# Optimization experiments

Hardware: AMD Instinct MI355X
Metric: run time of the kernel (lower is better)

## Reference

```python
import jax, jax.numpy as jnp
import numpy as np

B = 65536      # num_agents * num_processes
NUM = 16       # num_entities (landmarks tracked per agent)


def setup_inputs() -> dict:
    key = jax.random.key(0)
    k = jax.random.split(key, 6)
    value = jax.random.normal(k[0], (B, NUM * 2), jnp.float32)          # last abs positions
    vel = jax.random.normal(k[1], (B, NUM * 2), jnp.float32) * 0.1     # kalman velocities
    A = jax.random.normal(k[2], (B, NUM, 4, 4), jnp.float32) * 0.5
    P = A @ jnp.swapaxes(A, -1, -2) + jnp.eye(4, dtype=jnp.float32) * 0.1  # PSD covariances
    obs = jax.random.normal(k[3], (B, NUM * 2), jnp.float32)            # observed abs positions
    lm = jax.random.randint(k[4], (B, NUM), 0, 8, jnp.int32)            # last-mask age counters
    mask = jax.random.randint(k[5], (B, NUM), 0, 2, jnp.int32)          # current visibility
    return {"value": value, "vel": vel, "P": P, "obs": obs, "lm": lm, "mask": mask}


def _forward(value, vel, P, obs, lm, mask):
    Bn, two_num = value.shape
    num = two_num // 2
    # ---- _infer: constant-velocity predict (dt = 1). NOTE: original code builds Q
    # but never adds it to predicted_P, so we faithfully omit it too.
    Fm = jnp.array([[1., 0., 1., 0.],
                    [0., 1., 0., 1.],
                    [0., 0., 1., 0.],
                    [0., 0., 0., 1.]], jnp.float32)
    states = jnp.concatenate([value.reshape(Bn, num, 2), vel.reshape(Bn, num, 2)], axis=-1)  # [B,n,4]
    pred = jnp.einsum('ij,bnj->bni', Fm, states)                 # F @ state
    pP = jnp.einsum('ij,bnjk,lk->bnil', Fm, P, Fm)               # F P F^T  [B,n,4,4]
    lv = pred[..., :2]
    lvel = pred[..., 2:]
    obs2 = obs.reshape(Bn, num, 2)

    # ---- _merge_tensor: Kalman update with H = [[1,0,0,0],[0,1,0,0]], R = 1e-5 I
    R = jnp.float32(1e-5)
    S = pP[..., :2, :2] + R * jnp.eye(2, dtype=jnp.float32)      # [B,n,2,2]
    det = S[..., 0, 0] * S[..., 1, 1] - S[..., 0, 1] * S[..., 1, 0]
    Sinv = jnp.stack([jnp.stack([S[..., 1, 1], -S[..., 0, 1]], -1),
                      jnp.stack([-S[..., 1, 0], S[..., 0, 0]], -1)], -2) / det[..., None, None]
    K = jnp.einsum('bnij,bnjk->bnik', pP[..., :, :2], Sinv)      # P H^T S^-1  [B,n,4,2]
    y = obs2 - lv                                                # innovation
    upd = pred + jnp.einsum('bnij,bnj->bni', K, y)               # [B,n,4]
    Pn = pP - jnp.einsum('bnij,bnjk->bnik', K, pP[..., :2, :])   # (I - K H) P

    # ---- _fuse condition logic (faithful, including the original's rP bugs:
    # rP for cond2 and cond3b is never written -> stays zero)
    lmf = lm.astype(jnp.float32)
    mf = mask.astype(jnp.float32)
    c1 = (lmf == 0) & (mf == 0)
    c2 = (lmf == 0) & (mf != 0)
    c3 = (lmf != 0) & (mf == 0)
    c4 = (lmf != 0) & (mf != 0)
    c3a = c3 & (lmf <= 5)
    c3e, c4e, c3ae = c3[..., None], c4[..., None], c3a[..., None]
    rv = jnp.where(c4e, upd[..., :2], jnp.where(c3e, lv, obs2))
    rvel = jnp.where(c4e, upd[..., 2:], jnp.where(c3ae, lvel, 0.))
    rm = jnp.where(c2 | c4, 1., jnp.where(c3a, lmf + 1., 0.))
    diagP = jnp.diag(jnp.array([1., 1., 10., 10.], jnp.float32))
    rP = jnp.where(c1[..., None, None], diagP,
                   jnp.where(c3a[..., None, None], pP,
                             jnp.where(c4[..., None, None], Pn, 0.)))
    return rv.reshape(Bn, -1), rm, rvel.reshape(Bn, -1), rP


def reference(value, vel, P, obs, lm, mask):
    return _forward(value, vel, P, obs, lm, mask)
```

## Files before the change

### kernel.cpp

```cpp
#include <hip/hip_runtime.h>

#define NUM 16
#define TPB 256
#define PSTRIDE 20

__global__ __launch_bounds__(TPB) void kf_update_kernel(
    const float* __restrict__ value,
    const float* __restrict__ vel,
    const float* __restrict__ Pin,
    const float* __restrict__ obs,
    const int*   __restrict__ lm,
    const int*   __restrict__ mask,
    float* __restrict__ out,
    int Bn)
{
    __shared__ float sm[TPB * PSTRIDE];

    const int tid   = threadIdx.x;
    const int gtid  = blockIdx.x * TPB + tid;
    const int total = Bn * NUM;
    const long long blockBase = (long long)blockIdx.x * TPB;
    const bool active = gtid < total;

    {
        const float4* Pg = reinterpret_cast<const float4*>(Pin) + blockBase * 4;
        const long long limit = (long long)total * 4 - blockBase * 4;
        #pragma unroll
        for (int k = 0; k < 4; ++k) {
            const int g = tid + TPB * k;
            if (g < limit) {
                const float4 x = Pg[g];
                const int tr = g >> 2, part = g & 3;
                *reinterpret_cast<float4*>(&sm[tr * PSTRIDE + part * 4]) = x;
            }
        }
    }

    float2 v = make_float2(0.f, 0.f), u = v, o = v;
    int l = 0, m = 0;
    if (active) {
        v = reinterpret_cast<const float2*>(value)[gtid];
        u = reinterpret_cast<const float2*>(vel)[gtid];
        o = reinterpret_cast<const float2*>(obs)[gtid];
        l = lm[gtid];
        m = mask[gtid];
    }

    __syncthreads();

    float Pm[16];
    #pragma unroll
    for (int c = 0; c < 4; ++c) {
        const float4 x = *reinterpret_cast<const float4*>(&sm[tid * PSTRIDE + c * 4]);
        Pm[c * 4 + 0] = x.x; Pm[c * 4 + 1] = x.y;
        Pm[c * 4 + 2] = x.z; Pm[c * 4 + 3] = x.w;
    }

    const float p0 = v.x + u.x;
    const float p1 = v.y + u.y;
    const float p2 = u.x;
    const float p3 = u.y;

    float Q[4][4];
    #pragma unroll
    for (int j = 0; j < 4; ++j) {
        Q[0][j] = Pm[0 * 4 + j] + Pm[2 * 4 + j];
        Q[1][j] = Pm[1 * 4 + j] + Pm[3 * 4 + j];
        Q[2][j] = Pm[2 * 4 + j];
        Q[3][j] = Pm[3 * 4 + j];
    }
    float pP[4][4];
    #pragma unroll
    for (int i = 0; i < 4; ++i) {
        pP[i][0] = Q[i][0] + Q[i][2];
        pP[i][1] = Q[i][1] + Q[i][3];
        pP[i][2] = Q[i][2];
        pP[i][3] = Q[i][3];
    }

    const float S00 = pP[0][0] + 1e-5f;
    const float S01 = pP[0][1];
    const float S10 = pP[1][0];
    const float S11 = pP[1][1] + 1e-5f;
    const float det  = S00 * S11 - S01 * S10;
    const float rdet = 1.0f / det;

    float K0[4], K1[4];
    #pragma unroll
    for (int i = 0; i < 4; ++i) {
        K0[i] = (pP[i][0] * S11 - pP[i][1] * S10) * rdet;
        K1[i] = (pP[i][1] * S00 - pP[i][0] * S01) * rdet;
    }

    const float y0 = o.x - p0;
    const float y1 = o.y - p1;
    const float upd0 = p0 + K0[0] * y0 + K1[0] * y1;
    const float upd1 = p1 + K0[1] * y0 + K1[1] * y1;
    const float upd2 = p2 + K0[2] * y0 + K1[2] * y1;
    const float upd3 = p3 + K0[3] * y0 + K1[3] * y1;

    float Pn[4][4];
    #pragma unroll
    for (int i = 0; i < 4; ++i) {
        #pragma unroll
        for (int j = 0; j < 4; ++j) {
            Pn[i][j] = pP[i][j] - (K0[i] * pP[0][j] + K1[i] * pP[1][j]);
        }
    }

    const bool c1  = (l == 0) && (m == 0);
    const bool c2  = (l == 0) && (m != 0);
    const bool c3  = (l != 0) && (m == 0);
    const bool c4  = (l != 0) && (m != 0);
    const bool c3a = c3 && (l <= 5);

    const float rv0  = c4 ? upd0 : (c3 ? p0 : o.x);
    const float rv1  = c4 ? upd1 : (c3 ? p1 : o.y);
    const float rvl0 = c4 ? upd2 : (c3a ? p2 : 0.0f);
    const float rvl1 = c4 ? upd3 : (c3a ? p3 : 0.0f);
    const float rmv  = (c2 || c4) ? 1.0f : (c3a ? (float)(l + 1) : 0.0f);

    float* rv_out   = out;
    float* rm_out   = out + (size_t)Bn * 32;
    float* rvel_out = out + (size_t)Bn * 48;
    float* rP_out   = out + (size_t)Bn * 80;

    if (active) {
        reinterpret_cast<float2*>(rv_out)[gtid]   = make_float2(rv0, rv1);
        rm_out[gtid] = rmv;
        reinterpret_cast<float2*>(rvel_out)[gtid] = make_float2(rvl0, rvl1);
    }

    __syncthreads();

    #pragma unroll
    for (int i = 0; i < 4; ++i) {
        float e[4];
        #pragma unroll
        for (int j = 0; j < 4; ++j) {
            const float diag = (i == j) ? ((i < 2) ? 1.0f : 10.0f) : 0.0f;
            e[j] = c1 ? diag : (c3a ? pP[i][j] : (c4 ? Pn[i][j] : 0.0f));
        }
        *reinterpret_cast<float4*>(&sm[tid * PSTRIDE + i * 4]) =
            make_float4(e[0], e[1], e[2], e[3]);
    }

    __syncthreads();

    {
        float4* rPg = reinterpret_cast<float4*>(rP_out) + blockBase * 4;
        const long long limit = (long long)total * 4 - blockBase * 4;
        #pragma unroll
        for (int k = 0; k < 4; ++k) {
            const int g = tid + TPB * k;
            if (g < limit) {
                const int tr = g >> 2, part = g & 3;
                rPg[g] = *reinterpret_cast<const float4*>(&sm[tr * PSTRIDE + part * 4]);
            }
        }
    }
}

extern "C" void kernel_launch(void* const* d_in, const int* in_sizes, int n_in,
                              void* d_out, int out_size, void* d_ws, size_t ws_size,
                              hipStream_t stream) {
    const float* value = (const float*)d_in[0];
    const float* vel   = (const float*)d_in[1];
    const float* P     = (const float*)d_in[2];
    const float* obs   = (const float*)d_in[3];
    const int*   lm    = (const int*)d_in[4];
    const int*   mask  = (const int*)d_in[5];

    const int Bn    = in_sizes[0] / (2 * NUM);
    const int total = Bn * NUM;
    const int blocks = (total + TPB - 1) / TPB;

    kf_update_kernel<<<blocks, TPB, 0, stream>>>(
        value, vel, P, obs, lm, mask, (float*)d_out, Bn);
}
```

Measured before the change: 177.9 us.

## Split each track across four lanes using shuffles instead of shared-memory staging

Each 4x4 covariance is now spread over four lanes, one row per lane, so P loads and rP stores go straight to and from global memory as coalesced float4 accesses. This removes the shared-memory transpose and its barriers. The F P F^T products, the S matrix rows and the predicted positions are exchanged with sub-warp shuffles. Each thread handles two tracks (tiles) to keep enough loads in flight, and launch bounds ask for higher occupancy. In exchange, the small per-track loads and the stores of rv, rvel and rm are now done redundantly across lanes or as scalar stores, so those accesses are less efficient.

```diff
diff --git a/kernel.cpp b/kernel.cpp
--- a/kernel.cpp
+++ b/kernel.cpp
@@ -2,9 +2,11 @@
 
 #define NUM 16
 #define TPB 256
-#define PSTRIDE 20
+#define TILES 2
+#define TRACKS_PER_TILE (TPB / 4)
+#define TRACKS_PER_BLOCK (TRACKS_PER_TILE * TILES)
 
-__global__ __launch_bounds__(TPB) void kf_update_kernel(
+__global__ __launch_bounds__(TPB, 8) void kf_update_kernel(
     const float* __restrict__ value,
     const float* __restrict__ vel,
     const float* __restrict__ Pin,
@@ -14,150 +16,110 @@
     float* __restrict__ out,
     int Bn)
 {
-    __shared__ float sm[TPB * PSTRIDE];
+    const int tid = threadIdx.x;
+    const int r   = tid & 3;
+    const int sub = tid >> 2;
+    const int total = Bn * NUM;
 
-    const int tid   = threadIdx.x;
-    const int gtid  = blockIdx.x * TPB + tid;
-    const int total = Bn * NUM;
-    const long long blockBase = (long long)blockIdx.x * TPB;
-    const bool active = gtid < total;
+    float* __restrict__ rv_out   = out;
+    float* __restrict__ rm_out   = out + (size_t)Bn * 32;
+    float* __restrict__ rvel_out = out + (size_t)Bn * 48;
+    float* __restrict__ rP_out   = out + (size_t)Bn * 80;
 
-    {
-        const float4* Pg = reinterpret_cast<const float4*>(Pin) + blockBase * 4;
-        const long long limit = (long long)total * 4 - blockBase * 4;
-        #pragma unroll
-        for (int k = 0; k < 4; ++k) {
-            const int g = tid + TPB * k;
-            if (g < limit) {
-                const float4 x = Pg[g];
-                const int tr = g >> 2, part = g & 3;
-                *reinterpret_cast<float4*>(&sm[tr * PSTRIDE + part * 4]) = x;
-            }
-        }
+    const int base = blockIdx.x * TRACKS_PER_BLOCK + sub;
+
+    int    t[TILES];
+    bool   act[TILES];
+    float4 Pr[TILES];
+    float2 v2[TILES], u2[TILES], o2[TILES];
+    int    lv[TILES], mv[TILES];
+
+    #pragma unroll
+    for (int k = 0; k < TILES; ++k) {
+        t[k]   = base + k * TRACKS_PER_TILE;
+        act[k] = t[k] < total;
+        const int tc = act[k] ? t[k] : 0;
+        Pr[k] = reinterpret_cast<const float4*>(Pin)[(size_t)tc * 4 + r];
+        v2[k] = reinterpret_cast<const float2*>(value)[tc];
+        u2[k] = reinterpret_cast<const float2*>(vel)[tc];
+        o2[k] = reinterpret_cast<const float2*>(obs)[tc];
+        lv[k] = lm[tc];
+        mv[k] = mask[tc];
     }
 
-    float2 v = make_float2(0.f, 0.f), u = v, o = v;
-    int l = 0, m = 0;
-    if (active) {
-        v = reinterpret_cast<const float2*>(value)[gtid];
-        u = reinterpret_cast<const float2*>(vel)[gtid];
-        o = reinterpret_cast<const float2*>(obs)[gtid];
-        l = lm[gtid];
-        m = mask[gtid];
-    }
+    #pragma unroll
+    for (int k = 0; k < TILES; ++k) {
+        const float pr = (r == 0) ? (v2[k].x + u2[k].x)
+                       : (r == 1) ? (v2[k].y + u2[k].y)
+                       : (r == 2) ? u2[k].x
+                                  : u2[k].y;
 
-    __syncthreads();
+        float q0 = Pr[k].x, q1 = Pr[k].y, q2 = Pr[k].z, q3 = Pr[k].w;
+        const float x0 = __shfl_xor(q0, 2);
+        const float x1 = __shfl_xor(q1, 2);
+        const float x2 = __shfl_xor(q2, 2);
+        const float x3 = __shfl_xor(q3, 2);
+        if (r < 2) { q0 += x0; q1 += x1; q2 += x2; q3 += x3; }
 
-    float Pm[16];
-    #pragma unroll
-    for (int c = 0; c < 4; ++c) {
-        const float4 x = *reinterpret_cast<const float4*>(&sm[tid * PSTRIDE + c * 4]);
-        Pm[c * 4 + 0] = x.x; Pm[c * 4 + 1] = x.y;
-        Pm[c * 4 + 2] = x.z; Pm[c * 4 + 3] = x.w;
-    }
+        const float a0 = q0 + q2;
+        const float a1 = q1 + q3;
+        const float a2 = q2;
+        const float a3 = q3;
 
-    const float p0 = v.x + u.x;
-    const float p1 = v.y + u.y;
-    const float p2 = u.x;
-    const float p3 = u.y;
+        const float r00 = __shfl(a0, 0, 4), r01 = __shfl(a1, 0, 4);
+        const float r02 = __shfl(a2, 0, 4), r03 = __shfl(a3, 0, 4);
+        const float r10 = __shfl(a0, 1, 4), r11 = __shfl(a1, 1, 4);
+        const float r12 = __shfl(a2, 1, 4), r13 = __shfl(a3, 1, 4);
 
-    float Q[4][4];
-    #pragma unroll
-    for (int j = 0; j < 4; ++j) {
-        Q[0][j] = Pm[0 * 4 + j] + Pm[2 * 4 + j];
-        Q[1][j] = Pm[1 * 4 + j] + Pm[3 * 4 + j];
-        Q[2][j] = Pm[2 * 4 + j];
-        Q[3][j] = Pm[3 * 4 + j];
-    }
-    float pP[4][4];
-    #pragma unroll
-    for (int i = 0; i < 4; ++i) {
-        pP[i][0] = Q[i][0] + Q[i][2];
-        pP[i][1] = Q[i][1] + Q[i][3];
-        pP[i][2] = Q[i][2];
-        pP[i][3] = Q[i][3];
-    }
+        const float S00 = r00 + 1e-5f;
+        const float S01 = r01;
+        const float S10 = r10;
+        const float S11 = r11 + 1e-5f;
+        const float rdet = 1.0f / (S00 * S11 - S01 * S10);
 
-    const float S00 = pP[0][0] + 1e-5f;
-    const float S01 = pP[0][1];
-    const float S10 = pP[1][0];
-    const float S11 = pP[1][1] + 1e-5f;
-    const float det  = S00 * S11 - S01 * S10;
-    const float rdet = 1.0f / det;
+        const float K0 = (a0 * S11 - a1 * S10) * rdet;
+        const float K1 = (a1 * S00 - a0 * S01) * rdet;
 
-    float K0[4], K1[4];
-    #pragma unroll
-    for (int i = 0; i < 4; ++i) {
-        K0[i] = (pP[i][0] * S11 - pP[i][1] * S10) * rdet;
-        K1[i] = (pP[i][1] * S00 - pP[i][0] * S01) * rdet;
-    }
+        const float p0 = __shfl(pr, 0, 4);
+        const float p1 = __shfl(pr, 1, 4);
+        const float y0 = o2[k].x - p0;
+        const float y1 = o2[k].y - p1;
+        const float updr = pr + K0 * y0 + K1 * y1;
 
-    const float y0 = o.x - p0;
-    const float y1 = o.y - p1;
-    const float upd0 = p0 + K0[0] * y0 + K1[0] * y1;
-    const float upd1 = p1 + K0[1] * y0 + K1[1] * y1;
-    const float upd2 = p2 + K0[2] * y0 + K1[2] * y1;
-    const float upd3 = p3 + K0[3] * y0 + K1[3] * y1;
+        const float Pn0 = a0 - (K0 * r00 + K1 * r10);
+        const float Pn1 = a1 - (K0 * r01 + K1 * r11);
+        const float Pn2 = a2 - (K0 * r02 + K1 * r12);
+        const float Pn3 = a3 - (K0 * r03 + K1 * r13);
 
-    float Pn[4][4];
-    #pragma unroll
-    for (int i = 0; i < 4; ++i) {
-        #pragma unroll
-        for (int j = 0; j < 4; ++j) {
-            Pn[i][j] = pP[i][j] - (K0[i] * pP[0][j] + K1[i] * pP[1][j]);
+        const int  l  = lv[k], m = mv[k];
+        const bool c1  = (l == 0) && (m == 0);
+        const bool c3  = (l != 0) && (m == 0);
+        const bool c4  = (l != 0) && (m != 0);
+        const bool c3a = c3 && (l <= 5);
+
+        const float dv = (r < 2) ? 1.0f : 10.0f;
+        float4 e;
+        e.x = c1 ? ((r == 0) ? dv : 0.0f) : (c3a ? a0 : (c4 ? Pn0 : 0.0f));
+        e.y = c1 ? ((r == 1) ? dv : 0.0f) : (c3a ? a1 : (c4 ? Pn1 : 0.0f));
+        e.z = c1 ? ((r == 2) ? dv : 0.0f) : (c3a ? a2 : (c4 ? Pn2 : 0.0f));
+        e.w = c1 ? ((r == 3) ? dv : 0.0f) : (c3a ? a3 : (c4 ? Pn3 : 0.0f));
+        if (act[k])
+            reinterpret_cast<float4*>(rP_out)[(size_t)t[k] * 4 + r] = e;
+
+        float  sval;
+        float* sp;
+        if (r < 2) {
+            const float oc = (r == 0) ? o2[k].x : o2[k].y;
+            sval = c4 ? updr : (c3 ? pr : oc);
+            sp   = rv_out + (size_t)t[k] * 2 + r;
+        } else {
+            sval = c4 ? updr : (c3a ? pr : 0.0f);
+            sp   = rvel_out + (size_t)t[k] * 2 + (r - 2);
         }
-    }
+        if (act[k]) *sp = sval;
 
-    const bool c1  = (l == 0) && (m == 0);
-    const bool c2  = (l == 0) && (m != 0);
-    const bool c3  = (l != 0) && (m == 0);
-    const bool c4  = (l != 0) && (m != 0);
-    const bool c3a = c3 && (l <= 5);
-
-    const float rv0  = c4 ? upd0 : (c3 ? p0 : o.x);
-    const float rv1  = c4 ? upd1 : (c3 ? p1 : o.y);
-    const float rvl0 = c4 ? upd2 : (c3a ? p2 : 0.0f);
-    const float rvl1 = c4 ? upd3 : (c3a ? p3 : 0.0f);
-    const float rmv  = (c2 || c4) ? 1.0f : (c3a ? (float)(l + 1) : 0.0f);
-
-    float* rv_out   = out;
-    float* rm_out   = out + (size_t)Bn * 32;
-    float* rvel_out = out + (size_t)Bn * 48;
-    float* rP_out   = out + (size_t)Bn * 80;
-
-    if (active) {
-        reinterpret_cast<float2*>(rv_out)[gtid]   = make_float2(rv0, rv1);
-        rm_out[gtid] = rmv;
-        reinterpret_cast<float2*>(rvel_out)[gtid] = make_float2(rvl0, rvl1);
-    }
-
-    __syncthreads();
-
-    #pragma unroll
-    for (int i = 0; i < 4; ++i) {
-        float e[4];
-        #pragma unroll
-        for (int j = 0; j < 4; ++j) {
-            const float diag = (i == j) ? ((i < 2) ? 1.0f : 10.0f) : 0.0f;
-            e[j] = c1 ? diag : (c3a ? pP[i][j] : (c4 ? Pn[i][j] : 0.0f));
-        }
-        *reinterpret_cast<float4*>(&sm[tid * PSTRIDE + i * 4]) =
-            make_float4(e[0], e[1], e[2], e[3]);
-    }
-
-    __syncthreads();
-
-    {
-        float4* rPg = reinterpret_cast<float4*>(rP_out) + blockBase * 4;
-        const long long limit = (long long)total * 4 - blockBase * 4;
-        #pragma unroll
-        for (int k = 0; k < 4; ++k) {
-            const int g = tid + TPB * k;
-            if (g < limit) {
-                const int tr = g >> 2, part = g & 3;
-                rPg[g] = *reinterpret_cast<const float4*>(&sm[tr * PSTRIDE + part * 4]);
-            }
-        }
+        const float rmv = (m != 0) ? 1.0f : (c3a ? (float)(l + 1) : 0.0f);
+        if (act[k] && r == 0) rm_out[t[k]] = rmv;
     }
 }
 
@@ -171,9 +133,9 @@
     const int*   lm    = (const int*)d_in[4];
     const int*   mask  = (const int*)d_in[5];
 
-    const int Bn    = in_sizes[0] / (2 * NUM);
-    const int total = Bn * NUM;
-    const int blocks = (total + TPB - 1) / TPB;
+    const int Bn     = in_sizes[0] / (2 * NUM);
+    const int total  = Bn * NUM;
+    const int blocks = (total + TRACKS_PER_BLOCK - 1) / TRACKS_PER_BLOCK;
 
     kf_update_kernel<<<blocks, TPB, 0, stream>>>(
         value, vel, P, obs, lm, mask, (float*)d_out, Bn);
```

Result: faster. 174.3 us (-2.0%).
